# Performance work log

Measured on AMD Instinct MI355X. Metric: run time of the kernel, lower is better.

The kernel has to match this reference:

```python
import jax, jax.numpy as jnp
import numpy as np

EPS = 1e-5

def _conv(x, w, b, stride, pad):
    y = jax.lax.conv_general_dilated(
        x, w, window_strides=(stride, stride),
        padding=[(pad, pad), (pad, pad)],
        dimension_numbers=('NCHW', 'OIHW', 'NCHW'))
    return y + b.reshape(1, -1, 1, 1)

def _bn(x, gamma, beta):
    # training-mode batch norm: per-channel batch statistics over (N, H, W)
    mean = jnp.mean(x, axis=(0, 2, 3), keepdims=True)
    var = jnp.var(x, axis=(0, 2, 3), keepdims=True)
    xn = (x - mean) * jax.lax.rsqrt(var + EPS)
    return gamma.reshape(1, -1, 1, 1) * xn + beta.reshape(1, -1, 1, 1)

def setup_inputs() -> dict:
    key = jax.random.key(0)
    ks = jax.random.split(key, 8)
    N, Cin, H, W = 64, 1024, 14, 14
    P = 256                      # planes (bottleneck width)
    Cout = P * 4                 # expansion = 4 -> 1024
    def kaiming(k, shape):
        fan_in = shape[1] * shape[2] * shape[3]
        return jax.random.normal(k, shape, jnp.float32) * np.float32(np.sqrt(2.0 / fan_in))
    return {
        'x':  jax.random.normal(ks[0], (N, Cin, H, W), jnp.float32),
        'w1': kaiming(ks[1], (P, Cin, 1, 1)),  'b1': jnp.zeros((P,), jnp.float32),
        'g1': jnp.ones((P,), jnp.float32),     'be1': jnp.zeros((P,), jnp.float32),
        'w2': kaiming(ks[2], (P, P, 3, 3)),    'b2': jnp.zeros((P,), jnp.float32),
        'g2': jnp.ones((P,), jnp.float32),     'be2': jnp.zeros((P,), jnp.float32),
        'w3': kaiming(ks[3], (Cout, P, 1, 1)), 'b3': jnp.zeros((Cout,), jnp.float32),
        'g3': jnp.ones((Cout,), jnp.float32),  'be3': jnp.zeros((Cout,), jnp.float32),
        'residual_scale': jnp.zeros((1,), jnp.float32),
    }

def reference(x, w1, b1, g1, be1, w2, b2, g2, be2, w3, b3, g3, be3, residual_scale):
    out = jax.nn.relu(_bn(_conv(x, w1, b1, 1, 0), g1, be1))   # 1x1 reduce
    out = jax.nn.relu(_bn(_conv(out, w2, b2, 1, 1), g2, be2)) # 3x3
    out = _bn(_conv(out, w3, b3, 1, 0), g3, be3)              # 1x1 expand
    out = jax.nn.softplus(residual_scale)[0] * out            # scaled residual branch
    out = x + out                                             # identity shortcut (stride=1, Cin==Cout)
    return jax.nn.relu(out)
```

## Files before the change

kernel.cpp:

```cpp
#include <hip/hip_runtime.h>
#include <hip/hip_bf16.h>
#include <cstdint>

#define NB   64
#define CIN  1024
#define HWSP 196
#define MTOT 12544
#define PL   256
#define COUT 1024

using f32x4 = __attribute__((ext_vector_type(4))) float;
using s16x8 = __attribute__((ext_vector_type(8))) short;

static __device__ __forceinline__ short f2bf(float f) {
  union { __hip_bfloat16 h; short s; } u;
  u.h = __float2bfloat16(f);
  return u.s;
}
static __device__ __forceinline__ float bf2f(short s) {
  union { float f; unsigned u; } x;
  x.u = ((unsigned)(unsigned short)s) << 16;
  return x.f;
}

static __device__ __forceinline__ void gload16(const void* g, void* l) {
  __builtin_amdgcn_global_load_lds((const __attribute__((address_space(1))) void*)g,
                                   (__attribute__((address_space(3))) void*)l, 16, 0, 0);
}

__global__ __launch_bounds__(256) void k_prep(const float* __restrict__ x,
                                              const float* __restrict__ w1,
                                              const float* __restrict__ w2,
                                              const float* __restrict__ w3,
                                              short* __restrict__ xb,
                                              short* __restrict__ w1b,
                                              short* __restrict__ w2b,
                                              short* __restrict__ w3b,
                                              float* __restrict__ statszero) {
  const int bid = blockIdx.x;
  if (bid < 2048) {
    __shared__ float tile[32][197];
    const int n = bid >> 5;
    const int c0 = (bid & 31) * 32;
    for (int idx = threadIdx.x; idx < 32 * 196; idx += 256) {
      int cl = idx / 196, hw = idx % 196;
      tile[cl][hw] = x[((size_t)(n * CIN + c0 + cl)) * HWSP + hw];
    }
    __syncthreads();
    for (int idx = threadIdx.x; idx < 196 * 32; idx += 256) {
      int hw = idx >> 5, cl = idx & 31;
      xb[((size_t)(n * HWSP + hw)) * CIN + c0 + cl] = f2bf(tile[cl][hw]);
    }
  } else if (bid < 6400) {
    int i = (bid - 2048) * 256 + threadIdx.x;
    if (i < 262144) w1b[i] = f2bf(w1[i]);
    int j = i - 262144;
    if (j >= 0 && j < 589824) {
      int co = j / 2304, rem = j % 2304;
      int d = rem >> 8, ci = rem & 255;
      w2b[j] = f2bf(w2[((size_t)(co * 256 + ci)) * 9 + d]);
    }
    int k = i - 851968;
    if (k >= 0 && k < 262144) w3b[k] = f2bf(w3[k]);
  } else {
    for (int k = threadIdx.x; k < 3136; k += 256) statszero[k] = 0.f;
  }
}

static __device__ __forceinline__ int swz(int row, int k16) {
  return row * 128 + (((unsigned)(k16 ^ (row & 7))) << 4);
}

template <int MODE, int K>
__global__ __launch_bounds__(256) void gemm_kernel(const short* __restrict__ A,
                                                   const short* __restrict__ Bw,
                                                   const float* __restrict__ bias,
                                                   short* __restrict__ Yb,
                                                   float* __restrict__ st,
                                                   int Nc,
                                                   const short* __restrict__ zerobuf) {
  __shared__ __align__(16) char lds[2][32768];

  const int m0 = blockIdx.x * 128;
  const int n0 = blockIdx.y * 128;
  const int t = threadIdx.x;
  const int lane = t & 63, wid = t >> 6;
  const int wm = wid >> 1, wn = wid & 1;
  const int g = lane >> 4, r = lane & 15;
  constexpr int NKT = K >> 6;

  const short* aSrc[4];
  int aN[4], aH[4], aW[4], aCi[4];
  const short* bSrc[4];
#pragma unroll
  for (int q = 0; q < 4; ++q) {
    int chunk = t + q * 256;
    int row = chunk >> 3;
    int k16s = (chunk & 7) ^ (row & 7);
    if (MODE == 0) {
      aSrc[q] = A + (size_t)(m0 + row) * K + k16s * 8;
    } else {
      int m = m0 + row;
      int n_ = m / 196;
      int hw = m - n_ * 196;
      aN[q] = n_;
      aH[q] = hw / 14;
      aW[q] = hw - aH[q] * 14;
      aCi[q] = k16s * 8;
    }
    bSrc[q] = Bw + (size_t)(n0 + row) * K + k16s * 8;
  }

  auto stage = [&](int buf, int kt) {
    const int k0 = kt << 6;
    char* dA = &lds[buf][0];
    char* dB = &lds[buf][16384];
#pragma unroll
    for (int q = 0; q < 4; ++q) {
      const short* s;
      if (MODE == 0) {
        s = aSrc[q] + k0;
      } else {
        int d = kt >> 2;
        int dh = d / 3, dw = d - dh * 3;
        int hh = aH[q] + dh - 1, ww = aW[q] + dw - 1;
        s = ((unsigned)hh < 14u && (unsigned)ww < 14u)
                ? A + ((size_t)(aN[q] * 196 + hh * 14 + ww)) * 256 + (k0 & 255) + aCi[q]
                : zerobuf;
      }
      gload16(s, dA + (t + q * 256) * 16);
    }
#pragma unroll
    for (int q = 0; q < 4; ++q)
      gload16(bSrc[q] + k0, dB + (t + q * 256) * 16);
  };

  f32x4 acc[4][4] = {};
  auto compute = [&](int buf) {
    char* baseA = &lds[buf][0];
    char* baseB = &lds[buf][16384];
#pragma unroll
    for (int ks = 0; ks < 2; ++ks) {
      s16x8 af[4], bfr[4];
#pragma unroll
      for (int i = 0; i < 4; ++i)
        af[i] = *(const s16x8*)(baseA + swz(wm * 64 + i * 16 + r, ks * 4 + g));
#pragma unroll
      for (int j = 0; j < 4; ++j)
        bfr[j] = *(const s16x8*)(baseB + swz(wn * 64 + j * 16 + r, ks * 4 + g));
#pragma unroll
      for (int i = 0; i < 4; ++i)
#pragma unroll
        for (int j = 0; j < 4; ++j)
          acc[i][j] = __builtin_amdgcn_mfma_f32_16x16x32_bf16(af[i], bfr[j], acc[i][j], 0, 0, 0);
    }
  };

  stage(0, 0);
  int cur = 0;
#pragma unroll 1
  for (int kt = 0; kt < NKT - 1; ++kt) {
    stage(cur ^ 1, kt + 1);
    asm volatile("s_waitcnt vmcnt(8)" ::: "memory");
    __builtin_amdgcn_s_barrier();
    compute(cur);
    asm volatile("" ::: "memory");
    __builtin_amdgcn_s_barrier();
    cur ^= 1;
  }
  asm volatile("s_waitcnt vmcnt(0)" ::: "memory");
  __builtin_amdgcn_s_barrier();
  compute(cur);

#pragma unroll
  for (int j = 0; j < 4; ++j) {
    int col = n0 + wn * 64 + j * 16 + r;
    float bv = bias[col];
    float ps = 0.f, pq = 0.f;
#pragma unroll
    for (int i = 0; i < 4; ++i) {
      int row_base = m0 + wm * 64 + i * 16 + g * 4;
#pragma unroll
      for (int rr = 0; rr < 4; ++rr) {
        float v = acc[i][j][rr] + bv;
        ps += v;
        pq += v * v;
        Yb[(size_t)(row_base + rr) * Nc + col] = f2bf(v);
      }
    }
    ps += __shfl_xor(ps, 16);
    ps += __shfl_xor(ps, 32);
    pq += __shfl_xor(pq, 16);
    pq += __shfl_xor(pq, 32);
    if (lane < 16) {
      atomicAdd(&st[col], ps);
      atomicAdd(&st[Nc + col], pq);
    }
  }
}

__global__ __launch_bounds__(256) void k_apply(short* __restrict__ Yb,
                                               const float* __restrict__ st,
                                               const float* __restrict__ gamma,
                                               const float* __restrict__ beta) {
  __shared__ float lsc[256], lsh[256];
  const int t = threadIdx.x;
  {
    const float inv = 1.0f / 12544.0f;
    float mean = st[t] * inv;
    float var = st[256 + t] * inv - mean * mean;
    float s = gamma[t] * rsqrtf(var + 1e-5f);
    lsc[t] = s;
    lsh[t] = beta[t] - mean * s;
  }
  __syncthreads();
  size_t i8 = ((size_t)blockIdx.x * 256 + t) * 8;
  s16x8 v = *(const s16x8*)(Yb + i8);
  int c0 = (int)(i8 & 255);
#pragma unroll
  for (int e = 0; e < 8; ++e) {
    float f = bf2f(v[e]);
    v[e] = f2bf(fmaxf(lsc[c0 + e] * f + lsh[c0 + e], 0.f));
  }
  *(s16x8*)(Yb + i8) = v;
}

__global__ __launch_bounds__(256) void k_final(const float* __restrict__ x,
                                               const short* __restrict__ y3b,
                                               const float* __restrict__ st,
                                               const float* __restrict__ gamma,
                                               const float* __restrict__ beta,
                                               const float* __restrict__ rs,
                                               float* __restrict__ out) {
  __shared__ short ytile[64][198];
  __shared__ float lsc[64], lsh[64];
  const int n = blockIdx.x;
  const int co0 = blockIdx.y * 64;
  const int t = threadIdx.x;
  if (t < 64) {
    const float inv = 1.0f / 12544.0f;
    int c = co0 + t;
    float mean = st[c] * inv;
    float var = st[1024 + c] * inv - mean * mean;
    float s = gamma[c] * rsqrtf(var + 1e-5f);
    lsc[t] = s;
    lsh[t] = beta[c] - mean * s;
  }
#pragma unroll
  for (int iter = 0; iter < 49; ++iter) {
    int idx = iter * 256 + t;
    int hw = idx >> 6, c = idx & 63;
    ytile[c][hw] = y3b[((size_t)(n * 196 + hw)) * 1024 + co0 + c];
  }
  __syncthreads();
  float z = rs[0];
  float s = fmaxf(z, 0.f) + log1pf(expf(-fabsf(z)));
#pragma unroll
  for (int iter = 0; iter < 49; ++iter) {
    int idx = iter * 256 + t;
    int co = idx / 196, hw = idx - co * 196;
    size_t xi = ((size_t)(n * 1024 + co0 + co)) * 196 + hw;
    float v = bf2f(ytile[co][hw]);
    float o = x[xi] + s * (lsc[co] * v + lsh[co]);
    out[xi] = fmaxf(o, 0.f);
  }
}

extern "C" void kernel_launch(void* const* d_in, const int* in_sizes, int n_in,
                              void* d_out, int out_size, void* d_ws, size_t ws_size,
                              hipStream_t stream) {
  const float* x   = (const float*)d_in[0];
  const float* w1  = (const float*)d_in[1];
  const float* b1  = (const float*)d_in[2];
  const float* g1  = (const float*)d_in[3];
  const float* be1 = (const float*)d_in[4];
  const float* w2  = (const float*)d_in[5];
  const float* b2  = (const float*)d_in[6];
  const float* g2  = (const float*)d_in[7];
  const float* be2 = (const float*)d_in[8];
  const float* w3  = (const float*)d_in[9];
  const float* b3  = (const float*)d_in[10];
  const float* g3  = (const float*)d_in[11];
  const float* be3 = (const float*)d_in[12];
  const float* rs  = (const float*)d_in[13];
  float* out = (float*)d_out;
  char* ws = (char*)d_ws;

  size_t off = 0;
  auto alloc = [&](size_t bytes) {
    size_t o = off;
    off += (bytes + 255) & ~(size_t)255;
    return o;
  };
  short* xb  = (short*)(ws + alloc((size_t)MTOT * CIN * 2));
  short* w1b = (short*)(ws + alloc((size_t)262144 * 2));
  short* w2b = (short*)(ws + alloc((size_t)589824 * 2));
  short* w3b = (short*)(ws + alloc((size_t)262144 * 2));
  short* y1b = (short*)(ws + alloc((size_t)MTOT * PL * 2));
  short* y2b = (short*)(ws + alloc((size_t)MTOT * PL * 2));
  short* y3b = (short*)(ws + alloc((size_t)MTOT * COUT * 2));
  float* stats = (float*)(ws + alloc(12288 + 256));
  float* stat1 = stats, *stat2 = stats + 512, *stat3 = stats + 1024;
  short* zerobuf = (short*)(stats + 3072);

  k_prep<<<6401, 256, 0, stream>>>(x, w1, w2, w3, xb, w1b, w2b, w3b, stats);

  gemm_kernel<0, 1024><<<dim3(98, 2), 256, 0, stream>>>(xb, w1b, b1, y1b, stat1, 256, zerobuf);
  k_apply<<<1568, 256, 0, stream>>>(y1b, stat1, g1, be1);

  gemm_kernel<1, 2304><<<dim3(98, 2), 256, 0, stream>>>(y1b, w2b, b2, y2b, stat2, 256, zerobuf);
  k_apply<<<1568, 256, 0, stream>>>(y2b, stat2, g2, be2);

  gemm_kernel<0, 256><<<dim3(98, 8), 256, 0, stream>>>(y2b, w3b, b3, y3b, stat3, 1024, zerobuf);

  k_final<<<dim3(64, 16), 256, 0, stream>>>(x, y3b, stat3, g3, be3, rs, out);
}
```

Measured before the change: 122.6 us.

## Use 512-thread GEMM blocks, vectorize bf16 prep stores, read residual from bf16

The GEMM kernels are relaunched with 8 waves per block, each computing a 64x32 sub-tile of the 128x128 output tile, which halves per-wave accumulators and raises latency hiding. The input prep kernel converts to bf16 while staging in shared memory and writes 16-byte vector stores. The final kernel reads the identity shortcut from the bf16 copy of x instead of the fp32 input, cutting memory traffic at the cost of rounding the residual to bf16 precision.

```diff
diff --git a/kernel.cpp b/kernel.cpp
--- a/kernel.cpp
+++ b/kernel.cpp
@@ -39,17 +39,18 @@
                                               float* __restrict__ statszero) {
   const int bid = blockIdx.x;
   if (bid < 2048) {
-    __shared__ float tile[32][197];
+    __shared__ short tbf[196][40];
     const int n = bid >> 5;
     const int c0 = (bid & 31) * 32;
     for (int idx = threadIdx.x; idx < 32 * 196; idx += 256) {
       int cl = idx / 196, hw = idx % 196;
-      tile[cl][hw] = x[((size_t)(n * CIN + c0 + cl)) * HWSP + hw];
+      tbf[hw][cl] = f2bf(x[((size_t)(n * CIN + c0 + cl)) * HWSP + hw]);
     }
     __syncthreads();
-    for (int idx = threadIdx.x; idx < 196 * 32; idx += 256) {
-      int hw = idx >> 5, cl = idx & 31;
-      xb[((size_t)(n * HWSP + hw)) * CIN + c0 + cl] = f2bf(tile[cl][hw]);
+    for (int idx = threadIdx.x; idx < 784; idx += 256) {
+      int hw = idx >> 2, c8 = (idx & 3) << 3;
+      *(s16x8*)(xb + ((size_t)(n * HWSP + hw)) * CIN + c0 + c8) =
+          *(const s16x8*)(&tbf[hw][c8]);
     }
   } else if (bid < 6400) {
     int i = (bid - 2048) * 256 + threadIdx.x;
@@ -72,29 +73,29 @@
 }
 
 template <int MODE, int K>
-__global__ __launch_bounds__(256) void gemm_kernel(const short* __restrict__ A,
-                                                   const short* __restrict__ Bw,
-                                                   const float* __restrict__ bias,
-                                                   short* __restrict__ Yb,
-                                                   float* __restrict__ st,
-                                                   int Nc,
-                                                   const short* __restrict__ zerobuf) {
+__global__ __launch_bounds__(512) void gemm512(const short* __restrict__ A,
+                                               const short* __restrict__ Bw,
+                                               const float* __restrict__ bias,
+                                               short* __restrict__ Yb,
+                                               float* __restrict__ st,
+                                               int Nc,
+                                               const short* __restrict__ zerobuf) {
   __shared__ __align__(16) char lds[2][32768];
+  constexpr int NKT = K >> 6;
 
   const int m0 = blockIdx.x * 128;
   const int n0 = blockIdx.y * 128;
   const int t = threadIdx.x;
   const int lane = t & 63, wid = t >> 6;
-  const int wm = wid >> 1, wn = wid & 1;
+  const int wm = wid >> 2, wn = wid & 3;
   const int g = lane >> 4, r = lane & 15;
-  constexpr int NKT = K >> 6;
-
-  const short* aSrc[4];
-  int aN[4], aH[4], aW[4], aCi[4];
-  const short* bSrc[4];
-#pragma unroll
-  for (int q = 0; q < 4; ++q) {
-    int chunk = t + q * 256;
+
+  const short* aSrc[2];
+  int aN[2], aH[2], aW[2], aCi[2];
+  const short* bSrc[2];
+#pragma unroll
+  for (int q = 0; q < 2; ++q) {
+    int chunk = t + q * 512;
     int row = chunk >> 3;
     int k16s = (chunk & 7) ^ (row & 7);
     if (MODE == 0) {
@@ -116,7 +117,7 @@
     char* dA = &lds[buf][0];
     char* dB = &lds[buf][16384];
 #pragma unroll
-    for (int q = 0; q < 4; ++q) {
+    for (int q = 0; q < 2; ++q) {
       const short* s;
       if (MODE == 0) {
         s = aSrc[q] + k0;
@@ -128,30 +129,30 @@
                 ? A + ((size_t)(aN[q] * 196 + hh * 14 + ww)) * 256 + (k0 & 255) + aCi[q]
                 : zerobuf;
       }
-      gload16(s, dA + (t + q * 256) * 16);
-    }
-#pragma unroll
-    for (int q = 0; q < 4; ++q)
-      gload16(bSrc[q] + k0, dB + (t + q * 256) * 16);
+      gload16(s, dA + (t + q * 512) * 16);
+    }
+#pragma unroll
+    for (int q = 0; q < 2; ++q)
+      gload16(bSrc[q] + k0, dB + (t + q * 512) * 16);
   };
 
-  f32x4 acc[4][4] = {};
+  f32x4 acc[4][2] = {};
   auto compute = [&](int buf) {
     char* baseA = &lds[buf][0];
     char* baseB = &lds[buf][16384];
 #pragma unroll
     for (int ks = 0; ks < 2; ++ks) {
-      s16x8 af[4], bfr[4];
+      s16x8 af[4], bfr[2];
 #pragma unroll
       for (int i = 0; i < 4; ++i)
         af[i] = *(const s16x8*)(baseA + swz(wm * 64 + i * 16 + r, ks * 4 + g));
 #pragma unroll
-      for (int j = 0; j < 4; ++j)
-        bfr[j] = *(const s16x8*)(baseB + swz(wn * 64 + j * 16 + r, ks * 4 + g));
+      for (int j = 0; j < 2; ++j)
+        bfr[j] = *(const s16x8*)(baseB + swz(wn * 32 + j * 16 + r, ks * 4 + g));
 #pragma unroll
       for (int i = 0; i < 4; ++i)
 #pragma unroll
-        for (int j = 0; j < 4; ++j)
+        for (int j = 0; j < 2; ++j)
           acc[i][j] = __builtin_amdgcn_mfma_f32_16x16x32_bf16(af[i], bfr[j], acc[i][j], 0, 0, 0);
     }
   };
@@ -161,7 +162,7 @@
 #pragma unroll 1
   for (int kt = 0; kt < NKT - 1; ++kt) {
     stage(cur ^ 1, kt + 1);
-    asm volatile("s_waitcnt vmcnt(8)" ::: "memory");
+    asm volatile("s_waitcnt vmcnt(4)" ::: "memory");
     __builtin_amdgcn_s_barrier();
     compute(cur);
     asm volatile("" ::: "memory");
@@ -173,8 +174,8 @@
   compute(cur);
 
 #pragma unroll
-  for (int j = 0; j < 4; ++j) {
-    int col = n0 + wn * 64 + j * 16 + r;
+  for (int j = 0; j < 2; ++j) {
+    int col = n0 + wn * 32 + j * 16 + r;
     float bv = bias[col];
     float ps = 0.f, pq = 0.f;
 #pragma unroll
@@ -225,7 +226,7 @@
   *(s16x8*)(Yb + i8) = v;
 }
 
-__global__ __launch_bounds__(256) void k_final(const float* __restrict__ x,
+__global__ __launch_bounds__(256) void k_final(const short* __restrict__ xb,
                                                const short* __restrict__ y3b,
                                                const float* __restrict__ st,
                                                const float* __restrict__ gamma,
@@ -233,6 +234,7 @@
                                                const float* __restrict__ rs,
                                                float* __restrict__ out) {
   __shared__ short ytile[64][198];
+  __shared__ short xtile[64][198];
   __shared__ float lsc[64], lsh[64];
   const int n = blockIdx.x;
   const int co0 = blockIdx.y * 64;
@@ -250,7 +252,9 @@
   for (int iter = 0; iter < 49; ++iter) {
     int idx = iter * 256 + t;
     int hw = idx >> 6, c = idx & 63;
-    ytile[c][hw] = y3b[((size_t)(n * 196 + hw)) * 1024 + co0 + c];
+    size_t mrow = ((size_t)(n * 196 + hw)) * 1024 + co0 + c;
+    ytile[c][hw] = y3b[mrow];
+    xtile[c][hw] = xb[mrow];
   }
   __syncthreads();
   float z = rs[0];
@@ -261,7 +265,8 @@
     int co = idx / 196, hw = idx - co * 196;
     size_t xi = ((size_t)(n * 1024 + co0 + co)) * 196 + hw;
     float v = bf2f(ytile[co][hw]);
-    float o = x[xi] + s * (lsc[co] * v + lsh[co]);
+    float xv = bf2f(xtile[co][hw]);
+    float o = xv + s * (lsc[co] * v + lsh[co]);
     out[xi] = fmaxf(o, 0.f);
   }
 }
@@ -305,13 +310,13 @@
 
   k_prep<<<6401, 256, 0, stream>>>(x, w1, w2, w3, xb, w1b, w2b, w3b, stats);
 
-  gemm_kernel<0, 1024><<<dim3(98, 2), 256, 0, stream>>>(xb, w1b, b1, y1b, stat1, 256, zerobuf);
+  gemm512<0, 1024><<<dim3(98, 2), 512, 0, stream>>>(xb, w1b, b1, y1b, stat1, 256, zerobuf);
   k_apply<<<1568, 256, 0, stream>>>(y1b, stat1, g1, be1);
 
-  gemm_kernel<1, 2304><<<dim3(98, 2), 256, 0, stream>>>(y1b, w2b, b2, y2b, stat2, 256, zerobuf);
+  gemm512<1, 2304><<<dim3(98, 2), 512, 0, stream>>>(y1b, w2b, b2, y2b, stat2, 256, zerobuf);
   k_apply<<<1568, 256, 0, stream>>>(y2b, stat2, g2, be2);
 
-  gemm_kernel<0, 256><<<dim3(98, 8), 256, 0, stream>>>(y2b, w3b, b3, y3b, stat3, 1024, zerobuf);
-
-  k_final<<<dim3(64, 16), 256, 0, stream>>>(x, y3b, stat3, g3, be3, rs, out);
-}
+  gemm512<0, 256><<<dim3(98, 8), 512, 0, stream>>>(y2b, w3b, b3, y3b, stat3, 1024, zerobuf);
+
+  k_final<<<dim3(64, 16), 256, 0, stream>>>(xb, y3b, stat3, g3, be3, rs, out);
+}
```

Result: faster. 116.3 us (-5.2%).
